# Kernel optimization log

Hardware: AMD Instinct MI355X
Metric: run time of the kernel (lower is better)

## Reference

```python
import jax, jax.numpy as jnp
import numpy as np

FILTER_LENGTH = 1024
HOP_LENGTH = 512
CUTOFF = FILTER_LENGTH // 2 + 1  # 513
PAD_AMOUNT = FILTER_LENGTH // 2  # 512


def _make_forward_basis():
    # DFT matrix rows (real stacked over imag, up to Nyquist), windowed by periodic Hann.
    fb = np.fft.fft(np.eye(FILTER_LENGTH))
    fb = np.vstack([np.real(fb[:CUTOFF, :]), np.imag(fb[:CUTOFF, :])])  # [1026, 1024]
    n = np.arange(FILTER_LENGTH)
    # scipy get_window('hann', N, fftbins=True) == periodic Hann
    win = 0.5 * (1.0 - np.cos(2.0 * np.pi * n / FILTER_LENGTH))
    basis = (fb * win[None, :]).astype(np.float32)
    return basis[:, None, :]  # [out_ch=1026, in_ch=1, k=1024]


def setup_inputs() -> dict:
    key = jax.random.key(0)
    audio = jax.random.normal(key, (15360000,), dtype=jnp.float32)
    forward_basis = jnp.asarray(_make_forward_basis())
    return {"audio": audio, "forward_basis": forward_basis}


def reference(audio, forward_basis):
    # [L] -> [1, 1, L + 2*pad] with reflect padding
    x = jnp.pad(audio, (PAD_AMOUNT, PAD_AMOUNT), mode="reflect")[None, None, :]
    # Strided conv1d == windowed DFT per frame; output [1, 1026, n_frames]
    ft = jax.lax.conv_general_dilated(
        x,
        forward_basis,
        window_strides=(HOP_LENGTH,),
        padding="VALID",
        dimension_numbers=("NCH", "OIH", "NCH"),
    )
    real = ft[:, :CUTOFF, :]
    imag = ft[:, CUTOFF:, :]
    return real * real + imag * imag  # power spectrum [1, 513, n_frames]
```

## Files before the change

### kernel.cpp

```cpp
#include <hip/hip_runtime.h>

#define L_AUDIO 15360000
#define PADLEN  15361024
#define FRAMES  30001
#define CHP     513
#define NBAS    (1026*1024)

#define BM  128
#define BNP 64
#define BK  64

typedef __attribute__((ext_vector_type(8))) short short8;
typedef __attribute__((ext_vector_type(4))) float f32x4;

__device__ __forceinline__ unsigned short f2bf(float f) {
    unsigned int u = __float_as_uint(f);
    u += 0x7fffu + ((u >> 16) & 1u);
    return (unsigned short)(u >> 16);
}

__global__ __launch_bounds__(256) void prep_pad_k(const float* __restrict__ a,
                                                  unsigned short* __restrict__ pad) {
    long i = (long)blockIdx.x * blockDim.x + threadIdx.x;
    long p0 = i * 4;
    if (p0 >= 512 && p0 + 4 <= 512 + L_AUDIO) {
        const float4 v = *reinterpret_cast<const float4*>(a + (p0 - 512));
        ushort4 o;
        o.x = f2bf(v.x); o.y = f2bf(v.y); o.z = f2bf(v.z); o.w = f2bf(v.w);
        *reinterpret_cast<ushort4*>(pad + p0) = o;
    } else {
        for (int j = 0; j < 4; ++j) {
            long p = p0 + j;
            long src = p - 512;
            if (p < 512) src = 512 - p;
            else if (src >= L_AUDIO) src = 2L*L_AUDIO - 2 - src;
            pad[p] = f2bf(a[src]);
        }
    }
}

__global__ __launch_bounds__(256) void prep_bas_k(const float* __restrict__ b,
                                                  unsigned short* __restrict__ o) {
    long i = (long)blockIdx.x * blockDim.x + threadIdx.x;
    const float4 v = *reinterpret_cast<const float4*>(b + i * 4);
    ushort4 u;
    u.x = f2bf(v.x); u.y = f2bf(v.y); u.z = f2bf(v.z); u.w = f2bf(v.w);
    *reinterpret_cast<ushort4*>(o + i * 4) = u;
}

__global__ __launch_bounds__(256) void stft_gemm(const unsigned short* __restrict__ pad,
                                                 const unsigned short* __restrict__ bas,
                                                 float* __restrict__ out) {
    __shared__ unsigned short lsA[BM * BK];
    __shared__ unsigned short lsB[BM * BK];

    const int tid  = threadIdx.x;
    const int w    = tid >> 6;
    const int lane = tid & 63;
    const int l15  = lane & 15;
    const int lk   = lane >> 4;

    const int  c0 = blockIdx.x * BNP;
    const long t0 = (long)blockIdx.y * BM;

    const unsigned short* asrc[4];
    const unsigned short* bsrc[4];
    int ldsbase[4];
    #pragma unroll
    for (int j = 0; j < 4; ++j) {
        const int i = w * 4 + j;
        const int c = i * 64 + lane;
        const int row = c >> 3;
        const int chlog = (c & 7) ^ (row & 7);
        ldsbase[j] = i * 512;
        long t = t0 + row; if (t > FRAMES - 1) t = FRAMES - 1;
        asrc[j] = pad + t * 512 + chlog * 8;
        int ch = c0 + (row & 63); if (ch > 512) ch = 512;
        long brow = (row < 64) ? (long)ch : (long)(513 + ch);
        bsrc[j] = bas + brow * 1024 + chlog * 8;
    }

    f32x4 acc[2][8];
    #pragma unroll
    for (int m = 0; m < 2; ++m)
        #pragma unroll
        for (int n = 0; n < 8; ++n)
            acc[m][n] = (f32x4){0.f, 0.f, 0.f, 0.f};

    for (int kk = 0; kk < 1024; kk += BK) {
        if (kk) __syncthreads();
        #pragma unroll
        for (int j = 0; j < 4; ++j) {
            __builtin_amdgcn_global_load_lds(
                (const __attribute__((address_space(1))) unsigned int*)(asrc[j] + kk),
                (__attribute__((address_space(3))) unsigned int*)&lsA[ldsbase[j]],
                16, 0, 0);
            __builtin_amdgcn_global_load_lds(
                (const __attribute__((address_space(1))) unsigned int*)(bsrc[j] + kk),
                (__attribute__((address_space(3))) unsigned int*)&lsB[ldsbase[j]],
                16, 0, 0);
        }
        __syncthreads();

        #pragma unroll
        for (int s = 0; s < 2; ++s) {
            short8 af[2], bf[8];
            #pragma unroll
            for (int m = 0; m < 2; ++m) {
                const int r = w * 32 + m * 16 + l15;
                const int byt = (s * 64 + lk * 16) ^ ((r & 7) << 4);
                af[m] = *reinterpret_cast<const short8*>(
                    reinterpret_cast<const char*>(lsA) + r * 128 + byt);
            }
            #pragma unroll
            for (int n = 0; n < 8; ++n) {
                const int r = n * 16 + l15;
                const int byt = (s * 64 + lk * 16) ^ ((r & 7) << 4);
                bf[n] = *reinterpret_cast<const short8*>(
                    reinterpret_cast<const char*>(lsB) + r * 128 + byt);
            }
            #pragma unroll
            for (int m = 0; m < 2; ++m)
                #pragma unroll
                for (int n = 0; n < 8; ++n)
                    acc[m][n] = __builtin_amdgcn_mfma_f32_16x16x32_bf16(af[m], bf[n], acc[m][n], 0, 0, 0);
        }
    }

    const int tbase = (int)t0 + w * 32;
    #pragma unroll
    for (int m = 0; m < 2; ++m) {
        #pragma unroll
        for (int n = 0; n < 4; ++n) {
            const int ch = c0 + n * 16 + l15;
            if (ch >= CHP) continue;
            const long obase = (long)ch * FRAMES;
            #pragma unroll
            for (int r = 0; r < 4; ++r) {
                const int t = tbase + m * 16 + lk * 4 + r;
                if (t < FRAMES) {
                    const float re = acc[m][n][r], im = acc[m][n + 4][r];
                    out[obase + t] = re * re + im * im;
                }
            }
        }
    }
}

extern "C" void kernel_launch(void* const* d_in, const int* in_sizes, int n_in,
                              void* d_out, int out_size, void* d_ws, size_t ws_size,
                              hipStream_t stream) {
    const float* audio = (const float*)d_in[0];
    const float* basis = (const float*)d_in[1];
    float* out = (float*)d_out;

    unsigned short* pad = (unsigned short*)d_ws;
    unsigned short* bas = pad + PADLEN;

    prep_pad_k<<<PADLEN / 4 / 256, 256, 0, stream>>>(audio, pad);
    prep_bas_k<<<NBAS / 4 / 256, 256, 0, stream>>>(basis, bas);

    dim3 grid((CHP + BNP - 1) / BNP, (FRAMES + BM - 1) / BM);
    stft_gemm<<<grid, 256, 0, stream>>>(pad, bas, out);
}
```

Before: 132.2 us.

## Double-buffer LDS tiles and remap blocks to XCDs for frame locality

New measurement: 126.5 us. 1.04x faster.

```diff
diff --git a/kernel.cpp b/kernel.cpp
--- a/kernel.cpp
+++ b/kernel.cpp
@@ -9,6 +9,9 @@
 #define BM  128
 #define BNP 64
 #define BK  64
+#define NKT 16
+#define NCB 9
+#define NFB 235
 
 typedef __attribute__((ext_vector_type(8))) short short8;
 typedef __attribute__((ext_vector_type(4))) float f32x4;
@@ -51,17 +54,26 @@
 __global__ __launch_bounds__(256) void stft_gemm(const unsigned short* __restrict__ pad,
                                                  const unsigned short* __restrict__ bas,
                                                  float* __restrict__ out) {
-    __shared__ unsigned short lsA[BM * BK];
-    __shared__ unsigned short lsB[BM * BK];
+    __shared__ unsigned short lsA[2][BM * BK];
+    __shared__ unsigned short lsB[2][BM * BK];
+
+    const int bid = blockIdx.x;
+    const int xcd = bid & 7;
+    const int idx = bid >> 3;
+    const int nfb = (xcd < 3) ? 30 : 29;
+    if (idx >= nfb * NCB) return;
+    const int fstart = (xcd < 3) ? xcd * 30 : 90 + (xcd - 3) * 29;
+    const int fb = fstart + idx / NCB;
+    const int cb = idx % NCB;
+
+    const long t0 = (long)fb * BM;
+    const int  c0 = cb * BNP;
 
     const int tid  = threadIdx.x;
     const int w    = tid >> 6;
     const int lane = tid & 63;
     const int l15  = lane & 15;
     const int lk   = lane >> 4;
-
-    const int  c0 = blockIdx.x * BNP;
-    const long t0 = (long)blockIdx.y * BM;
 
     const unsigned short* asrc[4];
     const unsigned short* bsrc[4];
@@ -87,20 +99,35 @@
         for (int n = 0; n < 8; ++n)
             acc[m][n] = (f32x4){0.f, 0.f, 0.f, 0.f};
 
-    for (int kk = 0; kk < 1024; kk += BK) {
-        if (kk) __syncthreads();
-        #pragma unroll
-        for (int j = 0; j < 4; ++j) {
-            __builtin_amdgcn_global_load_lds(
-                (const __attribute__((address_space(1))) unsigned int*)(asrc[j] + kk),
-                (__attribute__((address_space(3))) unsigned int*)&lsA[ldsbase[j]],
-                16, 0, 0);
-            __builtin_amdgcn_global_load_lds(
-                (const __attribute__((address_space(1))) unsigned int*)(bsrc[j] + kk),
-                (__attribute__((address_space(3))) unsigned int*)&lsB[ldsbase[j]],
-                16, 0, 0);
+    #pragma unroll
+    for (int j = 0; j < 4; ++j) {
+        __builtin_amdgcn_global_load_lds(
+            (const __attribute__((address_space(1))) unsigned int*)asrc[j],
+            (__attribute__((address_space(3))) unsigned int*)&lsA[0][ldsbase[j]], 16, 0, 0);
+        __builtin_amdgcn_global_load_lds(
+            (const __attribute__((address_space(1))) unsigned int*)bsrc[j],
+            (__attribute__((address_space(3))) unsigned int*)&lsB[0][ldsbase[j]], 16, 0, 0);
+    }
+
+    for (int t = 0; t < NKT; ++t) {
+        const int cur = t & 1;
+        if (t + 1 < NKT) {
+            const int koff = (t + 1) * BK;
+            #pragma unroll
+            for (int j = 0; j < 4; ++j) {
+                __builtin_amdgcn_global_load_lds(
+                    (const __attribute__((address_space(1))) unsigned int*)(asrc[j] + koff),
+                    (__attribute__((address_space(3))) unsigned int*)&lsA[cur ^ 1][ldsbase[j]], 16, 0, 0);
+                __builtin_amdgcn_global_load_lds(
+                    (const __attribute__((address_space(1))) unsigned int*)(bsrc[j] + koff),
+                    (__attribute__((address_space(3))) unsigned int*)&lsB[cur ^ 1][ldsbase[j]], 16, 0, 0);
+            }
+            asm volatile("s_waitcnt vmcnt(8)" ::: "memory");
+        } else {
+            asm volatile("s_waitcnt vmcnt(0)" ::: "memory");
         }
-        __syncthreads();
+        __builtin_amdgcn_s_barrier();
+        asm volatile("" ::: "memory");
 
         #pragma unroll
         for (int s = 0; s < 2; ++s) {
@@ -110,14 +137,14 @@
                 const int r = w * 32 + m * 16 + l15;
                 const int byt = (s * 64 + lk * 16) ^ ((r & 7) << 4);
                 af[m] = *reinterpret_cast<const short8*>(
-                    reinterpret_cast<const char*>(lsA) + r * 128 + byt);
+                    reinterpret_cast<const char*>(lsA[cur]) + r * 128 + byt);
             }
             #pragma unroll
             for (int n = 0; n < 8; ++n) {
                 const int r = n * 16 + l15;
                 const int byt = (s * 64 + lk * 16) ^ ((r & 7) << 4);
                 bf[n] = *reinterpret_cast<const short8*>(
-                    reinterpret_cast<const char*>(lsB) + r * 128 + byt);
+                    reinterpret_cast<const char*>(lsB[cur]) + r * 128 + byt);
             }
             #pragma unroll
             for (int m = 0; m < 2; ++m)
@@ -125,6 +152,9 @@
                 for (int n = 0; n < 8; ++n)
                     acc[m][n] = __builtin_amdgcn_mfma_f32_16x16x32_bf16(af[m], bf[n], acc[m][n], 0, 0, 0);
         }
+
+        asm volatile("s_waitcnt lgkmcnt(0)" ::: "memory");
+        __builtin_amdgcn_s_barrier();
     }
 
     const int tbase = (int)t0 + w * 32;
@@ -160,6 +190,5 @@
     prep_pad_k<<<PADLEN / 4 / 256, 256, 0, stream>>>(audio, pad);
     prep_bas_k<<<NBAS / 4 / 256, 256, 0, stream>>>(basis, bas);
 
-    dim3 grid((CHP + BNP - 1) / BNP, (FRAMES + BM - 1) / BM);
-    stft_gemm<<<grid, 256, 0, stream>>>(pad, bas, out);
+    stft_gemm<<<8 * 270, 256, 0, stream>>>(pad, bas, out);
 }
```
